# Optimization experiments

Measured on AMD Instinct MI355X. Metric: run time of the kernel, lower is better.

The kernel has to match this reference:

```python
import jax, jax.numpy as jnp
import numpy as np

BN_EPS = 1e-5

def _resample_map(n_out):
    # out[..., i::7, j::7] = crop[..., min(i,5)::6, min(j,5)::6]
    # => output position p maps to crop position 6*(p//7) + min(p%7, 5)
    p = np.arange(n_out)
    return jnp.asarray((p // 7) * 6 + np.minimum(p % 7, 5), dtype=jnp.int32)


def setup_inputs() -> dict:
    key = jax.random.key(0)
    k = jax.random.split(key, 6)
    B, C, H, W = 32, 512, 56, 56
    C2, Cout = 2 * C, 256
    x = jax.random.normal(k[0], (B, C, H, W), dtype=jnp.float32)
    bn_gamma = jax.random.uniform(k[1], (C2,), dtype=jnp.float32, minval=0.5, maxval=1.5)
    bn_beta = jax.random.normal(k[2], (C2,), dtype=jnp.float32) * 0.1
    bn_mean = jax.random.normal(k[3], (C2,), dtype=jnp.float32) * 0.1
    bn_var = jax.random.uniform(k[4], (C2,), dtype=jnp.float32, minval=0.5, maxval=1.5)
    conv_w = jax.random.normal(k[5], (Cout, C2), dtype=jnp.float32) * (1.0 / np.sqrt(C2))
    return {"x": x, "bn_gamma": bn_gamma, "bn_beta": bn_beta,
            "bn_mean": bn_mean, "bn_var": bn_var, "conv_w": conv_w}


def reference(x, bn_gamma, bn_beta, bn_mean, bn_var, conv_w):
    # checkerboard resample: crop 56->48, expand back 48 -> 56 via separable gather
    crop = x[:, :, 4:-4, 4:-4]                      # [B,C,48,48]
    idx = _resample_map(56)                         # [56]
    up = crop[:, :, idx, :][:, :, :, idx]           # [B,C,56,56]
    cat = jnp.concatenate([x, up], axis=1)          # [B,2C,56,56]
    # origin block: BN (inference) -> ReLU -> 1x1 conv -> AvgPool 2x2 s2
    inv = (bn_gamma / jnp.sqrt(bn_var + BN_EPS))[None, :, None, None]
    h = (cat - bn_mean[None, :, None, None]) * inv + bn_beta[None, :, None, None]
    h = jax.nn.relu(h)
    y = jnp.einsum('bchw,oc->bohw', h, conv_w)      # 1x1 conv, [B,256,56,56]
    b, o, H, W = y.shape
    y = y.reshape(b, o, H // 2, 2, W // 2, 2).mean(axis=(3, 5))  # [B,256,28,28]
    return y
```

## Files before the change

### kernel.cpp

```cpp
#include <hip/hip_runtime.h>
#include <hip/hip_bf16.h>

typedef float  floatx4 __attribute__((ext_vector_type(4)));
typedef float  float4a __attribute__((ext_vector_type(4), aligned(4)));
typedef short  short8  __attribute__((ext_vector_type(8)));
typedef short  short4v __attribute__((ext_vector_type(4)));

#define NB   32
#define NC   512
#define NHW  3136

__device__ __forceinline__ int ridx(int p) {
    int q = p / 7;
    int r = p - q * 7;
    return q * 6 + (r < 5 ? r : 5);
}
__device__ __forceinline__ short f2bf(float f) {
    unsigned int x = __builtin_bit_cast(unsigned int, f);
    x += 0x7fffu + ((x >> 16) & 1u);
    return (short)(x >> 16);
}
__device__ __forceinline__ void gload_lds16(const void* g, void* l) {
    __builtin_amdgcn_global_load_lds(
        (const __attribute__((address_space(1))) unsigned int*)g,
        (__attribute__((address_space(3))) unsigned int*)l, 16, 0, 0);
}

__global__ __launch_bounds__(256)
void prep_kernel(const float* __restrict__ w,
                 const float* __restrict__ g_, const float* __restrict__ be_,
                 const float* __restrict__ mn_, const float* __restrict__ vr_,
                 short* __restrict__ wb, float* __restrict__ pbg)
{
    int id = (blockIdx.x * 256 + threadIdx.x) * 4;
    float4 v = *(const float4*)(w + id);
    short4v s;
    s[0] = f2bf(v.x); s[1] = f2bf(v.y); s[2] = f2bf(v.z); s[3] = f2bf(v.w);
    *(short4v*)(wb + id) = s;
    if (blockIdx.x == 0) {
        for (int c = threadIdx.x; c < 1024; c += 256) {
            float sc = g_[c] * rsqrtf(vr_[c] + 1e-5f);
            pbg[2 * c]     = sc;
            pbg[2 * c + 1] = be_[c] - mn_[c] * sc;
        }
    }
}

__global__ __launch_bounds__(256, 2)
void fused_bn_conv_pool(const float* __restrict__ x,
                        const float* __restrict__ pbg,
                        const short* __restrict__ wgt,
                        float* __restrict__ out)
{
    __shared__ char smem[65536];
    short* WtB[2] = { (short*)(smem),         (short*)(smem + 32768) };
    short* AtB[2] = { (short*)(smem + 16384), (short*)(smem + 49152) };
    float* ys = (float*)smem;

    const int t    = threadIdx.x;
    const int bx   = blockIdx.x;
    const int site = bx >> 1;
    const int nt   = bx & 1;
    const int b    = site / 28;
    const int ph   = site - b * 28;

    const int cc     = t & 7;
    const int mg     = t >> 3;
    const int m_base = mg * 4;
    const bool realm = (m_base < 112);
    const int rr = (m_base >= 56) ? 1 : 0;
    const int w0 = m_base - rr * 56;
    const int hs = 4 + ridx(2 * ph + rr);
    const int c0 = ridx(w0);
    const int offg = hs * 56 + 4 + c0;
    int d_[4];
#pragma unroll
    for (int j = 0; j < 4; ++j) d_[j] = ridx(w0 + j) - c0;
    const int xb   = b * NC * NHW;
    const int offd = 112 * ph + m_base;

    const int lid = t & 63;
    const int wv  = t >> 6;
    const int wo  = wv & 1;
    const int wm  = wv >> 1;
    const int col = lid & 15;
    const int q4  = lid >> 4;
    const int obw = wo * 64;
    const int mbw = wm * 64;
    const int sw  = col & 7;

    floatx4 acc[4][4];
#pragma unroll
    for (int i = 0; i < 4; ++i)
#pragma unroll
        for (int j = 0; j < 4; ++j)
            acc[i][j] = (floatx4){0.f, 0.f, 0.f, 0.f};

    const short* wrow = wgt + nt * 128 * 1024;

    float4a pf[8];
    float4  pp[4];

    auto load_pref = [&](int kc) {
        const int k0  = kc * 64;
        const int cb  = k0 + cc * 8;
#pragma unroll
        for (int ii = 0; ii < 4; ++ii) pp[ii] = *(const float4*)(pbg + cb * 2 + ii * 4);
        if (realm) {
            if (k0 < 512) {
#pragma unroll
                for (int i = 0; i < 8; ++i)
                    pf[i] = *(const float4a*)(x + xb + (cb + i) * NHW + offd);
            } else {
#pragma unroll
                for (int i = 0; i < 8; ++i)
                    pf[i] = *(const float4a*)(x + xb + (cb + i - 512) * NHW + offg);
            }
        }
    };

    load_pref(0);

    auto body = [&](int kc, short* Wt, short* At) {
        const int k0 = kc * 64;
#pragma unroll
        for (int it = 0; it < 4; ++it) {
            int q = it * 256 + t;
            int o = q >> 3, s = q & 7;
            gload_lds16(wrow + o * 1024 + k0 + ((s ^ (o & 7)) * 8), Wt + q * 8);
        }
        {
            const bool upper = (k0 >= 512);
            short8 vj[4];
#pragma unroll
            for (int j = 0; j < 4; ++j) vj[j] = (short8){0,0,0,0,0,0,0,0};
            if (realm) {
#pragma unroll
                for (int i = 0; i < 8; ++i) {
                    const float sc = pp[i >> 1][(i & 1) * 2];
                    const float sh = pp[i >> 1][(i & 1) * 2 + 1];
                    float vv[4];
                    if (!upper) {
#pragma unroll
                        for (int j = 0; j < 4; ++j) vv[j] = pf[i][j];
                    } else {
#pragma unroll
                        for (int j = 0; j < 4; ++j) {
                            int dd = d_[j];
                            float a = (dd >= 2) ? pf[i][2] : pf[i][0];
                            float bq = (dd >= 2) ? pf[i][3] : pf[i][1];
                            vv[j] = (dd & 1) ? bq : a;
                        }
                    }
#pragma unroll
                    for (int j = 0; j < 4; ++j)
                        vj[j][i] = f2bf(fmaxf(vv[j] * sc + sh, 0.f));
                }
            }
#pragma unroll
            for (int j = 0; j < 4; ++j) {
                int m = m_base + j;
                *(short8*)(At + m * 64 + ((cc ^ (m & 7)) * 8)) = vj[j];
            }
        }
        __syncthreads();

        if (kc < 15) load_pref(kc + 1);

#pragma unroll
        for (int ks = 0; ks < 2; ++ks) {
            const int cb = ks * 4 + q4;
            short8 af[4], bf[4];
#pragma unroll
            for (int of = 0; of < 4; ++of) {
                int row = obw + of * 16 + col;
                af[of] = *(const short8*)(Wt + row * 64 + ((cb ^ sw) * 8));
            }
#pragma unroll
            for (int mf = 0; mf < 4; ++mf) {
                int row = mbw + mf * 16 + col;
                bf[mf] = *(const short8*)(At + row * 64 + ((cb ^ sw) * 8));
            }
#pragma unroll
            for (int of = 0; of < 4; ++of)
#pragma unroll
                for (int mf = 0; mf < 4; ++mf)
                    acc[of][mf] = __builtin_amdgcn_mfma_f32_16x16x32_bf16(
                        af[of], bf[mf], acc[of][mf], 0, 0, 0);
        }
    };

    for (int kc2 = 0; kc2 < 16; kc2 += 2) {
        body(kc2,     WtB[0], AtB[0]);
        body(kc2 + 1, WtB[1], AtB[1]);
    }

    __syncthreads();

#pragma unroll
    for (int s = 0; s < 4; ++s) {
        if (wo == (s >> 1)) {
#pragma unroll
            for (int of2 = 0; of2 < 2; ++of2) {
                const int of  = (s & 1) * 2 + of2;
                const int olb = of2 * 16 + q4 * 4;
#pragma unroll
                for (int mf = 0; mf < 4; ++mf) {
                    const int m = mbw + mf * 16 + col;
#pragma unroll
                    for (int rg = 0; rg < 4; ++rg)
                        ys[(olb + rg) * 132 + m] = acc[of][mf][rg];
                }
            }
        }
        __syncthreads();
        for (int i = t; i < 896; i += 256) {
            int ol = i / 28;
            int pw = i - ol * 28;
            const float* yr = ys + ol * 132 + 2 * pw;
            float v = (yr[0] + yr[1] + yr[56] + yr[57]) * 0.25f;
            int og = nt * 128 + s * 32 + ol;
            out[((b * 256 + og) * 28 + ph) * 28 + pw] = v;
        }
        __syncthreads();
    }
}

extern "C" void kernel_launch(void* const* d_in, const int* in_sizes, int n_in,
                              void* d_out, int out_size, void* d_ws, size_t ws_size,
                              hipStream_t stream) {
    (void)in_sizes; (void)n_in; (void)out_size; (void)ws_size;
    const float* x  = (const float*)d_in[0];
    const float* g  = (const float*)d_in[1];
    const float* be = (const float*)d_in[2];
    const float* mn = (const float*)d_in[3];
    const float* vr = (const float*)d_in[4];
    const float* w  = (const float*)d_in[5];
    float* o   = (float*)d_out;
    short* wb  = (short*)d_ws;
    float* pbg = (float*)((char*)d_ws + 524288);

    prep_kernel<<<dim3(256), dim3(256), 0, stream>>>(w, g, be, mn, vr, wb, pbg);
    fused_bn_conv_pool<<<dim3(32 * 28 * 2), dim3(256), 0, stream>>>(x, pbg, wb, o);
}
```

Measured before the change: 411.3 us.

## Split fused BN-conv-pool block across 512 threads with halved per-thread work

Doubles the block size to 512 threads (8 waves), so each thread stages 2 spatial positions instead of 4. Each wave computes a 64x32 output tile instead of 64x64, which halves the accumulator registers. Loads become float2 and the checkerboard gather reduces to one select. The goal is more waves in flight to hide global-load latency. In exchange, the tighter launch bounds may force register spills, and each wave does fewer MFMAs per LDS fragment read, so LDS traffic per unit of compute rises.

```diff
diff --git a/kernel.cpp b/kernel.cpp
--- a/kernel.cpp
+++ b/kernel.cpp
@@ -2,7 +2,7 @@
 #include <hip/hip_bf16.h>
 
 typedef float  floatx4 __attribute__((ext_vector_type(4)));
-typedef float  float4a __attribute__((ext_vector_type(4), aligned(4)));
+typedef float  float2a __attribute__((ext_vector_type(2), aligned(4)));
 typedef short  short8  __attribute__((ext_vector_type(8)));
 typedef short  short4v __attribute__((ext_vector_type(4)));
 
@@ -46,7 +46,7 @@
     }
 }
 
-__global__ __launch_bounds__(256, 2)
+__global__ __launch_bounds__(512, 4)
 void fused_bn_conv_pool(const float* __restrict__ x,
                         const float* __restrict__ pbg,
                         const short* __restrict__ wgt,
@@ -66,16 +66,14 @@
 
     const int cc     = t & 7;
     const int mg     = t >> 3;
-    const int m_base = mg * 4;
+    const int m_base = mg * 2;
     const bool realm = (m_base < 112);
     const int rr = (m_base >= 56) ? 1 : 0;
     const int w0 = m_base - rr * 56;
     const int hs = 4 + ridx(2 * ph + rr);
     const int c0 = ridx(w0);
     const int offg = hs * 56 + 4 + c0;
-    int d_[4];
-#pragma unroll
-    for (int j = 0; j < 4; ++j) d_[j] = ridx(w0 + j) - c0;
+    const int d1 = ridx(w0 + 1) - c0;
     const int xb   = b * NC * NHW;
     const int offd = 112 * ph + m_base;
 
@@ -86,19 +84,19 @@
     const int col = lid & 15;
     const int q4  = lid >> 4;
     const int obw = wo * 64;
-    const int mbw = wm * 64;
+    const int mbw = wm * 32;
     const int sw  = col & 7;
 
-    floatx4 acc[4][4];
+    floatx4 acc[4][2];
 #pragma unroll
     for (int i = 0; i < 4; ++i)
 #pragma unroll
-        for (int j = 0; j < 4; ++j)
+        for (int j = 0; j < 2; ++j)
             acc[i][j] = (floatx4){0.f, 0.f, 0.f, 0.f};
 
     const short* wrow = wgt + nt * 128 * 1024;
 
-    float4a pf[8];
+    float2a pf[8];
     float4  pp[4];
 
     auto load_pref = [&](int kc) {
@@ -110,11 +108,11 @@
             if (k0 < 512) {
 #pragma unroll
                 for (int i = 0; i < 8; ++i)
-                    pf[i] = *(const float4a*)(x + xb + (cb + i) * NHW + offd);
+                    pf[i] = *(const float2a*)(x + xb + (cb + i) * NHW + offd);
             } else {
 #pragma unroll
                 for (int i = 0; i < 8; ++i)
-                    pf[i] = *(const float4a*)(x + xb + (cb + i - 512) * NHW + offg);
+                    pf[i] = *(const float2a*)(x + xb + (cb + i - 512) * NHW + offg);
             }
         }
     };
@@ -124,41 +122,30 @@
     auto body = [&](int kc, short* Wt, short* At) {
         const int k0 = kc * 64;
 #pragma unroll
-        for (int it = 0; it < 4; ++it) {
-            int q = it * 256 + t;
+        for (int it = 0; it < 2; ++it) {
+            int q = it * 512 + t;
             int o = q >> 3, s = q & 7;
             gload_lds16(wrow + o * 1024 + k0 + ((s ^ (o & 7)) * 8), Wt + q * 8);
         }
         {
             const bool upper = (k0 >= 512);
-            short8 vj[4];
-#pragma unroll
-            for (int j = 0; j < 4; ++j) vj[j] = (short8){0,0,0,0,0,0,0,0};
+            short8 vj[2];
+#pragma unroll
+            for (int j = 0; j < 2; ++j) vj[j] = (short8){0,0,0,0,0,0,0,0};
             if (realm) {
 #pragma unroll
                 for (int i = 0; i < 8; ++i) {
                     const float sc = pp[i >> 1][(i & 1) * 2];
                     const float sh = pp[i >> 1][(i & 1) * 2 + 1];
-                    float vv[4];
-                    if (!upper) {
-#pragma unroll
-                        for (int j = 0; j < 4; ++j) vv[j] = pf[i][j];
-                    } else {
-#pragma unroll
-                        for (int j = 0; j < 4; ++j) {
-                            int dd = d_[j];
-                            float a = (dd >= 2) ? pf[i][2] : pf[i][0];
-                            float bq = (dd >= 2) ? pf[i][3] : pf[i][1];
-                            vv[j] = (dd & 1) ? bq : a;
-                        }
-                    }
-#pragma unroll
-                    for (int j = 0; j < 4; ++j)
-                        vj[j][i] = f2bf(fmaxf(vv[j] * sc + sh, 0.f));
+                    float v0, v1;
+                    if (!upper) { v0 = pf[i][0]; v1 = pf[i][1]; }
+                    else        { v0 = pf[i][0]; v1 = d1 ? pf[i][1] : pf[i][0]; }
+                    vj[0][i] = f2bf(fmaxf(v0 * sc + sh, 0.f));
+                    vj[1][i] = f2bf(fmaxf(v1 * sc + sh, 0.f));
                 }
             }
 #pragma unroll
-            for (int j = 0; j < 4; ++j) {
+            for (int j = 0; j < 2; ++j) {
                 int m = m_base + j;
                 *(short8*)(At + m * 64 + ((cc ^ (m & 7)) * 8)) = vj[j];
             }
@@ -170,21 +157,21 @@
 #pragma unroll
         for (int ks = 0; ks < 2; ++ks) {
             const int cb = ks * 4 + q4;
-            short8 af[4], bf[4];
+            short8 af[4], bf[2];
 #pragma unroll
             for (int of = 0; of < 4; ++of) {
                 int row = obw + of * 16 + col;
                 af[of] = *(const short8*)(Wt + row * 64 + ((cb ^ sw) * 8));
             }
 #pragma unroll
-            for (int mf = 0; mf < 4; ++mf) {
+            for (int mf = 0; mf < 2; ++mf) {
                 int row = mbw + mf * 16 + col;
                 bf[mf] = *(const short8*)(At + row * 64 + ((cb ^ sw) * 8));
             }
 #pragma unroll
             for (int of = 0; of < 4; ++of)
 #pragma unroll
-                for (int mf = 0; mf < 4; ++mf)
+                for (int mf = 0; mf < 2; ++mf)
                     acc[of][mf] = __builtin_amdgcn_mfma_f32_16x16x32_bf16(
                         af[of], bf[mf], acc[of][mf], 0, 0, 0);
         }
@@ -205,7 +192,7 @@
                 const int of  = (s & 1) * 2 + of2;
                 const int olb = of2 * 16 + q4 * 4;
 #pragma unroll
-                for (int mf = 0; mf < 4; ++mf) {
+                for (int mf = 0; mf < 2; ++mf) {
                     const int m = mbw + mf * 16 + col;
 #pragma unroll
                     for (int rg = 0; rg < 4; ++rg)
@@ -214,7 +201,7 @@
             }
         }
         __syncthreads();
-        for (int i = t; i < 896; i += 256) {
+        for (int i = t; i < 896; i += 512) {
             int ol = i / 28;
             int pw = i - ol * 28;
             const float* yr = ys + ol * 132 + 2 * pw;
@@ -241,5 +228,5 @@
     float* pbg = (float*)((char*)d_ws + 524288);
 
     prep_kernel<<<dim3(256), dim3(256), 0, stream>>>(w, g, be, mn, vr, wb, pbg);
-    fused_bn_conv_pool<<<dim3(32 * 28 * 2), dim3(256), 0, stream>>>(x, pbg, wb, o);
-}
+    fused_bn_conv_pool<<<dim3(32 * 28 * 2), dim3(512), 0, stream>>>(x, pbg, wb, o);
+}
```

After: 484.5 us. 17.8% more time.
